# Optimization experiments

Hardware: AMD Instinct MI355X
Metric: run time of the kernel (lower is better)

Reference implementation:

```python
import jax, jax.numpy as jnp
import numpy as np

IN_FEATURES = 4096
OUT_FEATURES = 4096
N_TOKENS = 1024

@jax.custom_vjp
def binarize(w):
    # UnipolarSte.forward: (w > 0).float()
    return (w > 0).astype(w.dtype)

def _bin_fwd(w):
    return binarize(w), None

def _bin_bwd(_, g):
    # UnipolarSte.backward: F.hardtanh(grad_output) == clip(g, -1, 1)
    return (jnp.clip(g, -1.0, 1.0),)

binarize.defvjp(_bin_fwd, _bin_bwd)

def setup_inputs() -> dict:
    key = jax.random.key(0)
    kx, kw = jax.random.split(key)
    x = jax.random.normal(kx, (N_TOKENS, IN_FEATURES), dtype=jnp.float32)
    weight = jax.random.normal(kw, (OUT_FEATURES, IN_FEATURES), dtype=jnp.float32)
    scaling_factor = jnp.ones((OUT_FEATURES,), dtype=jnp.float32)
    return {"x": x, "weight": weight, "scaling_factor": scaling_factor}

def reference(x, weight, scaling_factor):
    w_b = binarize(weight)                      # [out, in] in {0,1}
    out = jnp.einsum('ni,oi->no', x, w_b)       # F.linear(x, w_b)
    # s_eff = round(clamp(s,1)).detach() - s.detach() + s
    s_round = jax.lax.stop_gradient(jnp.round(jnp.clip(scaling_factor, 1.0, None)))
    s_eff = s_round - jax.lax.stop_gradient(scaling_factor) + scaling_factor
    return out * s_eff[None, :]
```

## Files before the change

kernel.cpp:

```cpp
#include <hip/hip_runtime.h>

#define M_TOK 1024
#define NOUT  4096
#define KIN   4096

typedef __attribute__((ext_vector_type(8))) short bf16x8_t;
typedef __attribute__((ext_vector_type(4))) float f32x4_t;


__device__ __forceinline__ unsigned pack_bf16(float a, float b) {
  unsigned ua = __float_as_uint(a);
  unsigned ub = __float_as_uint(b);
  ua = (ua + 0x7FFFu + ((ua >> 16) & 1u)) >> 16;
  ub = (ub + 0x7FFFu + ((ub >> 16) & 1u)) >> 16;
  return ua | (ub << 16);
}

__global__ __launch_bounds__(256) void prep_wx(const float* __restrict__ w,
                                               unsigned short* __restrict__ bfrag,
                                               const float4* __restrict__ x4,
                                               uint4* __restrict__ xfrag) {
  __shared__ unsigned long long lbits[16][65];
  const int tid  = threadIdx.x;
  const int lane = tid & 63;
  const int wave = tid >> 6;

  if (blockIdx.x < 256) {
    const int n16 = blockIdx.x;
#pragma unroll 1
    for (int rr = 0; rr < 16; ++rr) {
      const float* wr = w + (size_t)(n16 * 16 + rr) * KIN + wave * 1024;
      unsigned long long mine = 0;
#pragma unroll 16
      for (int q = 0; q < 16; ++q) {
        float v = wr[q * 64 + lane];
        unsigned long long m = __ballot(v > 0.f);
        if (lane == q) mine = m;
      }
      if (lane < 16) lbits[rr][wave * 16 + lane] = mine;
    }
    __syncthreads();
#pragma unroll
    for (int it = 0; it < 16; ++it) {
      const int idx = it * 256 + tid;
      const int l = idx & 63, kt = idx >> 6;
      const unsigned long long w64 = lbits[l & 15][kt];
      const int quad = l >> 4;
      const unsigned b0 = (unsigned)(w64 >> (quad * 8)) & 0xFFu;
      const unsigned b1 = (unsigned)(w64 >> (quad * 8 + 32)) & 0xFFu;
      bfrag[(size_t)n16 * 4096 + idx] = (unsigned short)(b0 | (b1 << 8));
    }
  } else {
    const unsigned t = (blockIdx.x - 256) * 256 + tid;
    const int l = t & 63;
    const unsigned f = t >> 6;
    const int m16 = f >> 7, k32 = f & 127;
    const int row = m16 * 16 + (l & 15);
    const int c4  = k32 * 8 + (l >> 4) * 2;
    const float4* p = x4 + (size_t)row * (KIN / 4) + c4;
    float4 a = p[0], b = p[1];
    uint4 o;
    o.x = pack_bf16(a.x, a.y);
    o.y = pack_bf16(a.z, a.w);
    o.z = pack_bf16(b.x, b.y);
    o.w = pack_bf16(b.z, b.w);
    xfrag[t] = o;
  }
}

__global__ __launch_bounds__(256, 2) void gemm_bin_kernel(
    const unsigned short* __restrict__ Xf,
    const unsigned short* __restrict__ Bf,
    const float* __restrict__ sf,
    float* __restrict__ C) {
  const int tid  = threadIdx.x;
  const int lane = tid & 63;
  const int wave = tid >> 6;
  const int quad = lane >> 4;
  const int l16  = lane & 15;
  const unsigned bid = blockIdx.x;
  const int xcd = bid & 7, idx = bid >> 3;
  const int m0 = (xcd * 2 + (idx >> 5)) * 64;
  const int n0 = (idx & 31) * 128;
  const int wn = wave * 32;
  const int m16b = m0 >> 4;
  const int n16b = (n0 + wn) >> 4;

  const uint4* Xf4 = (const uint4*)Xf;

  f32x4_t acc[4][2];
#pragma unroll
  for (int i = 0; i < 4; ++i)
#pragma unroll
    for (int j = 0; j < 2; ++j)
      acc[i][j] = (f32x4_t){0.f, 0.f, 0.f, 0.f};

  uint4 a[4][4][2];
  unsigned b[4][2];

  auto LOAD = [&](int u, int kt) {
#pragma unroll
    for (int i = 0; i < 4; ++i)
#pragma unroll
      for (int ks = 0; ks < 2; ++ks)
        a[u][i][ks] = Xf4[((size_t)(m16b + i) * 128 + kt * 2 + ks) * 64 + lane];
#pragma unroll
    for (int j = 0; j < 2; ++j)
      b[u][j] = (unsigned)Bf[((n16b + j) * 64 + kt) * 64 + lane];
  };

  auto COMP = [&](int u) {
#pragma unroll
    for (int j = 0; j < 2; ++j)
#pragma unroll
      for (int ks = 0; ks < 2; ++ks) {
        const unsigned br = b[u][j];
        union { unsigned u32[4]; bf16x8_t v; } ex;
#pragma unroll
        for (int p = 0; p < 4; ++p)
          ex.u32[p] = ((br << (14 - 8 * ks - 2 * p)) |
                       (br << (29 - 8 * ks - 2 * p))) & 0x40004000u;
#pragma unroll
        for (int i = 0; i < 4; ++i) {
          union { uint4 q; bf16x8_t v; } av;
          av.q = a[u][i][ks];
          acc[i][j] = __builtin_amdgcn_mfma_f32_16x16x32_bf16(av.v, ex.v, acc[i][j], 0, 0, 0);
        }
      }
  };

  LOAD(0, 0);
  LOAD(1, 1);
  for (int kt = 0; kt < 64; kt += 4) {
    LOAD(2, kt + 2);
    COMP(0);
    LOAD(3, kt + 3);
    COMP(1);
    if (kt + 4 < 64) LOAD(0, kt + 4);
    COMP(2);
    if (kt + 5 < 64) LOAD(1, kt + 5);
    COMP(3);
  }

#pragma unroll
  for (int j = 0; j < 2; ++j) {
    const int n = n0 + wn + j * 16 + l16;
    const float s = rintf(fmaxf(sf[n], 1.0f)) * 0.5f;
#pragma unroll
    for (int i = 0; i < 4; ++i) {
      const int mr = m0 + i * 16 + quad * 4;
#pragma unroll
      for (int r = 0; r < 4; ++r)
        C[(size_t)(mr + r) * NOUT + n] = acc[i][j][r] * s;
    }
  }
}

extern "C" void kernel_launch(void* const* d_in, const int* in_sizes, int n_in,
                              void* d_out, int out_size, void* d_ws, size_t ws_size,
                              hipStream_t stream) {
  const float* x  = (const float*)d_in[0];
  const float* w  = (const float*)d_in[1];
  const float* sf = (const float*)d_in[2];
  float* out = (float*)d_out;

  unsigned short* Bfrag = (unsigned short*)d_ws;
  unsigned short* Xfrag = (unsigned short*)((char*)d_ws + (4u << 20));

  prep_wx<<<2304, 256, 0, stream>>>(w, Bfrag, (const float4*)x, (uint4*)Xfrag);
  gemm_bin_kernel<<<512, 256, 0, stream>>>(Xfrag, Bfrag, sf, out);
}
```

Measured before the change: 159.1 us.

## Pre-spread weight bits in prep, halve GEMM M tile, raise occupancy

The weight prep kernel is split across four blocks per 16-row group and now writes 32-bit pre-spread bit patterns, so the GEMM inner loop needs a single shift-and-mask per fragment word instead of two shifts and an or. The GEMM tile shrinks from 64 to 32 rows, the prefetch depth drops from four stages to two, and launch bounds rise to four blocks per SM with twice as many blocks. This trades register-level latency hiding and A/B reuse for more occupancy and parallelism, and it doubles the size of the B workspace read.

After: 154.9 us. 2.6% less time.

```diff
diff --git a/kernel.cpp b/kernel.cpp
--- a/kernel.cpp
+++ b/kernel.cpp
@@ -16,42 +16,53 @@
   return ua | (ub << 16);
 }
 
+__device__ __forceinline__ unsigned spread_bits(unsigned br) {
+  unsigned U = 0;
+#pragma unroll
+  for (int e = 0; e < 8; ++e)
+    U |= (((br >> (2 * e)) & 1u) << (14 - 2 * e)) |
+         (((br >> (2 * e + 1)) & 1u) << (30 - 2 * e));
+  return U;
+}
+
 __global__ __launch_bounds__(256) void prep_wx(const float* __restrict__ w,
-                                               unsigned short* __restrict__ bfrag,
+                                               unsigned* __restrict__ bfrag32,
                                                const float4* __restrict__ x4,
                                                uint4* __restrict__ xfrag) {
-  __shared__ unsigned long long lbits[16][65];
+  __shared__ unsigned long long lbits[16][17];
   const int tid  = threadIdx.x;
   const int lane = tid & 63;
   const int wave = tid >> 6;
 
-  if (blockIdx.x < 256) {
-    const int n16 = blockIdx.x;
+  if (blockIdx.x < 1024) {
+    const int n16 = blockIdx.x >> 2;
+    const int kq  = blockIdx.x & 3;
 #pragma unroll 1
     for (int rr = 0; rr < 16; ++rr) {
-      const float* wr = w + (size_t)(n16 * 16 + rr) * KIN + wave * 1024;
+      const float* wr = w + (size_t)(n16 * 16 + rr) * KIN + kq * 1024 + wave * 256;
       unsigned long long mine = 0;
-#pragma unroll 16
-      for (int q = 0; q < 16; ++q) {
+#pragma unroll
+      for (int q = 0; q < 4; ++q) {
         float v = wr[q * 64 + lane];
         unsigned long long m = __ballot(v > 0.f);
         if (lane == q) mine = m;
       }
-      if (lane < 16) lbits[rr][wave * 16 + lane] = mine;
+      if (lane < 4) lbits[rr][wave * 4 + lane] = mine;
     }
     __syncthreads();
 #pragma unroll
-    for (int it = 0; it < 16; ++it) {
+    for (int it = 0; it < 4; ++it) {
       const int idx = it * 256 + tid;
-      const int l = idx & 63, kt = idx >> 6;
-      const unsigned long long w64 = lbits[l & 15][kt];
+      const int l = idx & 63, ktl = idx >> 6;
+      const unsigned long long w64 = lbits[l & 15][ktl];
       const int quad = l >> 4;
       const unsigned b0 = (unsigned)(w64 >> (quad * 8)) & 0xFFu;
       const unsigned b1 = (unsigned)(w64 >> (quad * 8 + 32)) & 0xFFu;
-      bfrag[(size_t)n16 * 4096 + idx] = (unsigned short)(b0 | (b1 << 8));
+      const unsigned br = b0 | (b1 << 8);
+      bfrag32[((size_t)n16 * 64 + kq * 16 + ktl) * 64 + l] = spread_bits(br);
     }
   } else {
-    const unsigned t = (blockIdx.x - 256) * 256 + tid;
+    const unsigned t = (blockIdx.x - 1024) * 256 + tid;
     const int l = t & 63;
     const unsigned f = t >> 6;
     const int m16 = f >> 7, k32 = f & 127;
@@ -68,9 +79,9 @@
   }
 }
 
-__global__ __launch_bounds__(256, 2) void gemm_bin_kernel(
+__global__ __launch_bounds__(256, 4) void gemm_bin_kernel(
     const unsigned short* __restrict__ Xf,
-    const unsigned short* __restrict__ Bf,
+    const unsigned* __restrict__ Bf32,
     const float* __restrict__ sf,
     float* __restrict__ C) {
   const int tid  = threadIdx.x;
@@ -80,74 +91,68 @@
   const int l16  = lane & 15;
   const unsigned bid = blockIdx.x;
   const int xcd = bid & 7, idx = bid >> 3;
-  const int m0 = (xcd * 2 + (idx >> 5)) * 64;
+  const int m0 = (xcd * 4 + (idx >> 5)) * 32;
   const int n0 = (idx & 31) * 128;
-  const int wn = wave * 32;
   const int m16b = m0 >> 4;
-  const int n16b = (n0 + wn) >> 4;
+  const int n16b = (n0 + wave * 32) >> 4;
 
   const uint4* Xf4 = (const uint4*)Xf;
 
-  f32x4_t acc[4][2];
+  f32x4_t acc[2][2];
 #pragma unroll
-  for (int i = 0; i < 4; ++i)
+  for (int i = 0; i < 2; ++i)
 #pragma unroll
     for (int j = 0; j < 2; ++j)
       acc[i][j] = (f32x4_t){0.f, 0.f, 0.f, 0.f};
 
-  uint4 a[4][4][2];
-  unsigned b[4][2];
+  uint4 a[2][2][2];
+  unsigned b[2][2];
 
   auto LOAD = [&](int u, int kt) {
 #pragma unroll
-    for (int i = 0; i < 4; ++i)
+    for (int i = 0; i < 2; ++i)
 #pragma unroll
       for (int ks = 0; ks < 2; ++ks)
         a[u][i][ks] = Xf4[((size_t)(m16b + i) * 128 + kt * 2 + ks) * 64 + lane];
 #pragma unroll
     for (int j = 0; j < 2; ++j)
-      b[u][j] = (unsigned)Bf[((n16b + j) * 64 + kt) * 64 + lane];
+      b[u][j] = Bf32[((n16b + j) * 64 + kt) * 64 + lane];
   };
 
   auto COMP = [&](int u) {
 #pragma unroll
-    for (int j = 0; j < 2; ++j)
+    for (int j = 0; j < 2; ++j) {
+      const unsigned U = b[u][j];
 #pragma unroll
       for (int ks = 0; ks < 2; ++ks) {
-        const unsigned br = b[u][j];
         union { unsigned u32[4]; bf16x8_t v; } ex;
 #pragma unroll
         for (int p = 0; p < 4; ++p)
-          ex.u32[p] = ((br << (14 - 8 * ks - 2 * p)) |
-                       (br << (29 - 8 * ks - 2 * p))) & 0x40004000u;
+          ex.u32[p] = (U << (2 * (ks * 4 + p))) & 0x40004000u;
 #pragma unroll
-        for (int i = 0; i < 4; ++i) {
+        for (int i = 0; i < 2; ++i) {
           union { uint4 q; bf16x8_t v; } av;
           av.q = a[u][i][ks];
           acc[i][j] = __builtin_amdgcn_mfma_f32_16x16x32_bf16(av.v, ex.v, acc[i][j], 0, 0, 0);
         }
       }
+    }
   };
 
   LOAD(0, 0);
-  LOAD(1, 1);
-  for (int kt = 0; kt < 64; kt += 4) {
-    LOAD(2, kt + 2);
+  for (int kt = 0; kt < 64; kt += 2) {
+    LOAD(1, kt + 1);
     COMP(0);
-    LOAD(3, kt + 3);
+    if (kt + 2 < 64) LOAD(0, kt + 2);
     COMP(1);
-    if (kt + 4 < 64) LOAD(0, kt + 4);
-    COMP(2);
-    if (kt + 5 < 64) LOAD(1, kt + 5);
-    COMP(3);
   }
 
 #pragma unroll
   for (int j = 0; j < 2; ++j) {
-    const int n = n0 + wn + j * 16 + l16;
+    const int n = n0 + wave * 32 + j * 16 + l16;
     const float s = rintf(fmaxf(sf[n], 1.0f)) * 0.5f;
 #pragma unroll
-    for (int i = 0; i < 4; ++i) {
+    for (int i = 0; i < 2; ++i) {
       const int mr = m0 + i * 16 + quad * 4;
 #pragma unroll
       for (int r = 0; r < 4; ++r)
@@ -164,9 +169,9 @@
   const float* sf = (const float*)d_in[2];
   float* out = (float*)d_out;
 
-  unsigned short* Bfrag = (unsigned short*)d_ws;
-  unsigned short* Xfrag = (unsigned short*)((char*)d_ws + (4u << 20));
+  unsigned*       Bfrag32 = (unsigned*)d_ws;
+  unsigned short* Xfrag   = (unsigned short*)((char*)d_ws + (4u << 20));
 
-  prep_wx<<<2304, 256, 0, stream>>>(w, Bfrag, (const float4*)x, (uint4*)Xfrag);
-  gemm_bin_kernel<<<512, 256, 0, stream>>>(Xfrag, Bfrag, sf, out);
+  prep_wx<<<3072, 256, 0, stream>>>(w, Bfrag32, (const float4*)x, (uint4*)Xfrag);
+  gemm_bin_kernel<<<1024, 256, 0, stream>>>(Xfrag, Bfrag32, sf, out);
 }
```
